# Optimization experiments

Measured on AMD Instinct MI355X. Metric: run time of the kernel, lower is better.

Reference implementation:

```python
import jax, jax.numpy as jnp
import numpy as np

N_NODES = 50000

def setup_inputs() -> dict:
    key = jax.random.key(0)
    k1, k2, k3, k4, k5 = jax.random.split(key, 5)
    x = jax.random.normal(k1, (50000, 128), dtype=jnp.float32)
    weight = jax.random.normal(k2, (128, 32), dtype=jnp.float32) * (np.sqrt(6.0 / (128 + 32)))
    edge_src = jax.random.randint(k3, (1600000,), 0, N_NODES, dtype=jnp.int32)
    edge_dst = jax.random.randint(k4, (1600000,), 0, N_NODES, dtype=jnp.int32)
    edge_weight = jax.random.uniform(k5, (1600000,), dtype=jnp.float32)
    return {"x": x, "weight": weight, "edge_src": edge_src,
            "edge_dst": edge_dst, "edge_weight": edge_weight}

def reference(x, weight, edge_src, edge_dst, edge_weight):
    # h = x @ W  (dense GEMM)
    h = x @ weight                                   # [N, out]
    # out = spmm(adj, h): gather h rows at src, scale by edge weight,
    # scatter-add into dst rows (COO SpMM).
    msgs = edge_weight[:, None] * h[edge_src]        # [E, out]
    out = jax.ops.segment_sum(msgs, edge_dst, num_segments=N_NODES)
    return out
```

## Files before the change

kernel.cpp:

```cpp
#include <hip/hip_runtime.h>
#include <hip/hip_bf16.h>
#include <stdint.h>

#define N_NODES   50000
#define K_DIM     128
#define OUT_DIM   32
#define N_EDGES   1600000
#define NBKT      782
#define CAP       3072
#define AFIT      16
#define FB        ((N_EDGES + 256*AFIT - 1) / (256*AFIT))
#define GB        ((N_NODES + 63) / 64)

__global__ __launch_bounds__(256) void zero_cursor(int* __restrict__ cursor) {
    for (int i = threadIdx.x; i < NBKT; i += 256) cursor[i] = 0;
}

__global__ __launch_bounds__(256) void gemm_fill(const float* __restrict__ x,
                                                 const float* __restrict__ w,
                                                 __hip_bfloat16* __restrict__ h,
                                                 const int*   __restrict__ esrc,
                                                 const int*   __restrict__ edst,
                                                 const float* __restrict__ ew,
                                                 int*         __restrict__ cursor,
                                                 uint64_t*    __restrict__ pairs) {
    __shared__ __align__(16) char smem[50176];
    const int t = threadIdx.x;

    if (blockIdx.x < FB) {
        int*      cnt   = (int*)smem;
        int*      wbase = (int*)(smem + 3200);
        int*      scr   = (int*)(smem + 6400);
        uint16_t* rkA   = (uint16_t*)(smem + 7424);
        uint64_t* stg   = (uint64_t*)(smem + 17408);

        for (int i = t; i < 800; i += 256) cnt[i] = 0;
        __syncthreads();

        uint32_t lo[AFIT], hi[AFIT];
        uint16_t rk[AFIT];
        const int base = blockIdx.x * 256 * AFIT;
        #pragma unroll
        for (int k = 0; k < AFIT; ++k) {
            const int e = base + k * 256 + t;
            if (e < N_EDGES) {
                const uint32_t s = (uint32_t)esrc[e];
                const uint32_t d = (uint32_t)edst[e];
                lo[k] = (d << 16) | s;
                hi[k] = __float_as_uint(ew[e]);
                rk[k] = (uint16_t)atomicAdd(&cnt[d >> 6], 1);
            } else {
                lo[k] = 0xffffffffu;
            }
        }
        __syncthreads();
        for (int i = t; i < NBKT; i += 256) {
            const int c = cnt[i];
            if (c) wbase[i] = atomicAdd(&cursor[i], c);
        }
        __syncthreads();
        int v0[4]; int lsum = 0;
        #pragma unroll
        for (int j = 0; j < 4; ++j) { v0[j] = cnt[t * 4 + j] * ((t * 4 + j) < 800); lsum += v0[j]; }
        scr[t] = lsum;
        __syncthreads();
        #pragma unroll
        for (int d = 1; d < 256; d <<= 1) {
            const int a = (t >= d) ? scr[t - d] : 0;
            __syncthreads();
            scr[t] += a;
            __syncthreads();
        }
        int run = scr[t] - lsum;
        #pragma unroll
        for (int j = 0; j < 4; ++j) {
            if (t * 4 + j < 800) { const int c = v0[j]; cnt[t * 4 + j] = run; run += c; }
        }
        __syncthreads();
        #pragma unroll
        for (int k = 0; k < AFIT; ++k) {
            if (lo[k] != 0xffffffffu) {
                const int b = (int)(lo[k] >> 22);
                const int i = cnt[b] + (int)rk[k];
                stg[i] = ((uint64_t)hi[k] << 32) | lo[k];
                rkA[i] = rk[k];
            }
        }
        __syncthreads();
        const int total = min(4096, N_EDGES - base);
        for (int i = t; i < total; i += 256) {
            const uint64_t p = stg[i];
            const int b    = (int)((p >> 22) & 0x3ff);
            const int gpos = wbase[b] + (int)rkA[i];
            if (gpos < CAP)
                pairs[(size_t)b * CAP + gpos] = p;
        }
    } else {
        float*  wlds = (float*)smem;
        float4* wl4  = (float4*)smem;
        float4* xl4  = (float4*)(smem + 16384);

        const float4* wg4 = reinterpret_cast<const float4*>(w);
        #pragma unroll
        for (int i = 0; i < 4; ++i) wl4[i * 256 + t] = wg4[i * 256 + t];

        const int row0 = (blockIdx.x - FB) * 64;
        const long long gbase4 = (long long)row0 * (K_DIM / 4);
        const long long gmax4  = (long long)N_NODES * (K_DIM / 4);
        const float4* xg4 = reinterpret_cast<const float4*>(x);
        #pragma unroll
        for (int i = 0; i < 8; ++i) {
            const int idx = i * 256 + t;
            const int row = idx >> 5;
            const int k4  = idx & 31;
            const long long gi = gbase4 + idx;
            xl4[row * 33 + k4] = (gi < gmax4) ? xg4[gi]
                                              : make_float4(0.f, 0.f, 0.f, 0.f);
        }
        __syncthreads();

        const int cg = t & 15;
        const int rg = t >> 4;
        const float2* w2 = reinterpret_cast<const float2*>(wlds);

        float acc[4][2] = {{0.f,0.f},{0.f,0.f},{0.f,0.f},{0.f,0.f}};
        #pragma unroll 4
        for (int k4 = 0; k4 < K_DIM / 4; ++k4) {
            const int k = k4 * 4;
            const float2 wv0 = w2[(k + 0) * 16 + cg];
            const float2 wv1 = w2[(k + 1) * 16 + cg];
            const float2 wv2 = w2[(k + 2) * 16 + cg];
            const float2 wv3 = w2[(k + 3) * 16 + cg];
            #pragma unroll
            for (int r = 0; r < 4; ++r) {
                const float4 xv = xl4[(rg * 4 + r) * 33 + k4];
                acc[r][0] += xv.x * wv0.x + xv.y * wv1.x + xv.z * wv2.x + xv.w * wv3.x;
                acc[r][1] += xv.x * wv0.y + xv.y * wv1.y + xv.z * wv2.y + xv.w * wv3.y;
            }
        }
        uint32_t* h32 = reinterpret_cast<uint32_t*>(h);
        #pragma unroll
        for (int r = 0; r < 4; ++r) {
            const int row = row0 + rg * 4 + r;
            if (row < N_NODES) {
                __hip_bfloat16 b0 = __float2bfloat16(acc[r][0]);
                __hip_bfloat16 b1 = __float2bfloat16(acc[r][1]);
                const uint32_t u0 = *reinterpret_cast<uint16_t*>(&b0);
                const uint32_t u1 = *reinterpret_cast<uint16_t*>(&b1);
                h32[row * 16 + cg] = u0 | (u1 << 16);
            }
        }
    }
}

__global__ __launch_bounds__(512) void sort_pull(const int*      __restrict__ cursor,
                                                 const uint64_t* __restrict__ pairs,
                                                 const __hip_bfloat16* __restrict__ h,
                                                 float*          __restrict__ out) {
    __shared__ uint64_t stg[CAP];
    __shared__ int lcnt[64];
    __shared__ int loff[65];
    const int b    = blockIdx.x;
    const int t    = threadIdx.x;
    const size_t beg = (size_t)b * CAP;
    const int cnt  = min(cursor[b], CAP);
    const int wv   = t >> 6;
    const int lane = t & 63;
    const int col  = lane & 31;
    const int half = lane >> 5;

    if (t < 64) lcnt[t] = 0;
    __syncthreads();

    uint64_t pl[6];
    int      pr[6];
    #pragma unroll
    for (int k = 0; k < 6; ++k) {
        const int i = t + k * 512;
        if (i < cnt) {
            const uint64_t p = pairs[beg + i];
            const int nl = (int)((p >> 16) & 63);
            pl[k] = p;
            pr[k] = (nl << 12) | atomicAdd(&lcnt[nl], 1);
        } else {
            pr[k] = -1;
        }
    }
    __syncthreads();
    if (t < 64) {
        const int v = lcnt[t];
        int p = v;
        #pragma unroll
        for (int d = 1; d < 64; d <<= 1) {
            const int n = __shfl_up(p, d, 64);
            if (t >= d) p += n;
        }
        loff[t] = p - v;
        if (t == 63) loff[64] = p;
    }
    __syncthreads();
    #pragma unroll
    for (int k = 0; k < 6; ++k) {
        if (pr[k] >= 0)
            stg[loff[pr[k] >> 12] + (pr[k] & 0xfff)] = pl[k];
    }
    __syncthreads();

    for (int nl = wv * 8; nl < wv * 8 + 8; ++nl) {
        const int node = (b << 6) + nl;
        if (node >= N_NODES) break;
        const int jb = loff[nl], je = loff[nl + 1];
        float acc = 0.f;
        int j = jb + half;
        for (; j + 6 < je; j += 8) {
            const uint64_t p0 = stg[j];
            const uint64_t p1 = stg[j + 2];
            const uint64_t p2 = stg[j + 4];
            const uint64_t p3 = stg[j + 6];
            const float a0 = __bfloat162float(h[(size_t)(p0 & 0xffffu) * OUT_DIM + col]);
            const float a1 = __bfloat162float(h[(size_t)(p1 & 0xffffu) * OUT_DIM + col]);
            const float a2 = __bfloat162float(h[(size_t)(p2 & 0xffffu) * OUT_DIM + col]);
            const float a3 = __bfloat162float(h[(size_t)(p3 & 0xffffu) * OUT_DIM + col]);
            acc += __uint_as_float((uint32_t)(p0 >> 32)) * a0;
            acc += __uint_as_float((uint32_t)(p1 >> 32)) * a1;
            acc += __uint_as_float((uint32_t)(p2 >> 32)) * a2;
            acc += __uint_as_float((uint32_t)(p3 >> 32)) * a3;
        }
        for (; j < je; j += 2) {
            const uint64_t p = stg[j];
            acc += __uint_as_float((uint32_t)(p >> 32)) *
                   __bfloat162float(h[(size_t)(p & 0xffffu) * OUT_DIM + col]);
        }
        acc += __shfl_xor(acc, 32, 64);
        if (half == 0) out[(size_t)node * OUT_DIM + col] = acc;
    }
}

__global__ __launch_bounds__(256) void gemm_only(const float* __restrict__ x,
                                                 const float* __restrict__ w,
                                                 __hip_bfloat16* __restrict__ h) {
    __shared__ float wlds[K_DIM * OUT_DIM];
    const int t = threadIdx.x;
    #pragma unroll
    for (int i = 0; i < (K_DIM * OUT_DIM) / 256; ++i)
        wlds[i * 256 + t] = w[i * 256 + t];
    __syncthreads();
    const int row = blockIdx.x * 8 + (t >> 5);
    const int col = t & 31;
    if (row >= N_NODES) return;
    const float4* x4 = reinterpret_cast<const float4*>(x + (size_t)row * K_DIM);
    float acc = 0.f;
    #pragma unroll
    for (int k4 = 0; k4 < K_DIM / 4; ++k4) {
        float4 xv = x4[k4];
        const int k = k4 * 4;
        acc += xv.x * wlds[(k + 0) * OUT_DIM + col] + xv.y * wlds[(k + 1) * OUT_DIM + col]
             + xv.z * wlds[(k + 2) * OUT_DIM + col] + xv.w * wlds[(k + 3) * OUT_DIM + col];
    }
    h[(size_t)row * OUT_DIM + col] = __float2bfloat16(acc);
}

__global__ __launch_bounds__(256) void scatter_kernel(const int*   __restrict__ esrc,
                                                      const int*   __restrict__ edst,
                                                      const float* __restrict__ ew,
                                                      const __hip_bfloat16* __restrict__ h,
                                                      float*       out) {
    const long long gid = (long long)blockIdx.x * blockDim.x + threadIdx.x;
    const int e   = (int)(gid >> 5);
    const int col = (int)(gid & 31);
    if (e >= N_EDGES) return;
    atomicAdd(out + (size_t)edst[e] * OUT_DIM + col,
              ew[e] * __bfloat162float(h[(size_t)esrc[e] * OUT_DIM + col]));
}

extern "C" void kernel_launch(void* const* d_in, const int* in_sizes, int n_in,
                              void* d_out, int out_size, void* d_ws, size_t ws_size,
                              hipStream_t stream) {
    const float* x    = (const float*)d_in[0];
    const float* w    = (const float*)d_in[1];
    const int*   esrc = (const int*)d_in[2];
    const int*   edst = (const int*)d_in[3];
    const float* ew   = (const float*)d_in[4];
    float*       out  = (float*)d_out;

    const size_t PAIRS_B = (size_t)NBKT * CAP * 8;
    const size_t H_B     = (size_t)N_NODES * OUT_DIM * 2;
    const size_t CUR_B   = (size_t)NBKT * 4;
    const size_t REQ     = PAIRS_B + H_B + CUR_B;

    uint64_t*        pairs  = (uint64_t*)d_ws;
    __hip_bfloat16*  h      = (__hip_bfloat16*)((char*)d_ws + PAIRS_B);
    int*             cursor = (int*)((char*)d_ws + PAIRS_B + H_B);

    if (ws_size >= REQ) {
        zero_cursor<<<1, 256, 0, stream>>>(cursor);
        gemm_fill<<<FB + GB, 256, 0, stream>>>(x, w, h, esrc, edst, ew, cursor, pairs);
        sort_pull<<<NBKT, 512, 0, stream>>>(cursor, pairs, h, out);
    } else {
        __hip_bfloat16* hf = (__hip_bfloat16*)d_ws;
        (void)hipMemsetAsync(d_out, 0, (size_t)out_size * sizeof(float), stream);
        gemm_only<<<(N_NODES + 7) / 8, 256, 0, stream>>>(x, w, hf);
        const long long total = (long long)N_EDGES * OUT_DIM;
        scatter_kernel<<<(int)((total + 255) / 256), 256, 0, stream>>>(esrc, edst, ew, hf, out);
    }
}
```

Baseline: 63.41 us.

## Use bf16 MFMA for the dense GEMM and shrink edge-binning tiles

Replaces the scalar FP32 FMA GEMM in the fused gemm_fill kernel with bf16 MFMA 16x16x32 instructions. x and W are converted to bf16 into padded LDS tiles first. The edge-binning blocks now process 8 edges per thread instead of 16, which doubles the number of binning blocks. Each edge's in-bucket rank is now recomputed from the prefix offsets instead of being stored in a separate LDS array. The shared memory footprint drops, which may allow more blocks per CU. In exchange, inputs are rounded to bf16 before the multiply, which lowers GEMM precision, and more blocks issue atomics on the global cursor.

```diff
diff --git a/kernel.cpp b/kernel.cpp
--- a/kernel.cpp
+++ b/kernel.cpp
@@ -8,9 +8,13 @@
 #define N_EDGES   1600000
 #define NBKT      782
 #define CAP       3072
-#define AFIT      16
+#define AFIT      8
 #define FB        ((N_EDGES + 256*AFIT - 1) / (256*AFIT))
 #define GB        ((N_NODES + 63) / 64)
+#define XSTR      136
+
+typedef __attribute__((ext_vector_type(8))) short bf16x8;
+typedef __attribute__((ext_vector_type(4))) float f32x4;
 
 __global__ __launch_bounds__(256) void zero_cursor(int* __restrict__ cursor) {
     for (int i = threadIdx.x; i < NBKT; i += 256) cursor[i] = 0;
@@ -24,15 +28,14 @@
                                                  const float* __restrict__ ew,
                                                  int*         __restrict__ cursor,
                                                  uint64_t*    __restrict__ pairs) {
-    __shared__ __align__(16) char smem[50176];
+    __shared__ __align__(16) char smem[26112];
     const int t = threadIdx.x;
 
     if (blockIdx.x < FB) {
         int*      cnt   = (int*)smem;
         int*      wbase = (int*)(smem + 3200);
         int*      scr   = (int*)(smem + 6400);
-        uint16_t* rkA   = (uint16_t*)(smem + 7424);
-        uint64_t* stg   = (uint64_t*)(smem + 17408);
+        uint64_t* stg   = (uint64_t*)(smem + 7424);
 
         for (int i = t; i < 800; i += 256) cnt[i] = 0;
         __syncthreads();
@@ -61,7 +64,7 @@
         __syncthreads();
         int v0[4]; int lsum = 0;
         #pragma unroll
-        for (int j = 0; j < 4; ++j) { v0[j] = cnt[t * 4 + j] * ((t * 4 + j) < 800); lsum += v0[j]; }
+        for (int j = 0; j < 4; ++j) { v0[j] = (t * 4 + j < 800) ? cnt[t * 4 + j] : 0; lsum += v0[j]; }
         scr[t] = lsum;
         __syncthreads();
         #pragma unroll
@@ -81,73 +84,72 @@
         for (int k = 0; k < AFIT; ++k) {
             if (lo[k] != 0xffffffffu) {
                 const int b = (int)(lo[k] >> 22);
-                const int i = cnt[b] + (int)rk[k];
-                stg[i] = ((uint64_t)hi[k] << 32) | lo[k];
-                rkA[i] = rk[k];
+                stg[cnt[b] + (int)rk[k]] = ((uint64_t)hi[k] << 32) | lo[k];
             }
         }
         __syncthreads();
-        const int total = min(4096, N_EDGES - base);
+        const int total = min(256 * AFIT, N_EDGES - base);
         for (int i = t; i < total; i += 256) {
             const uint64_t p = stg[i];
             const int b    = (int)((p >> 22) & 0x3ff);
-            const int gpos = wbase[b] + (int)rkA[i];
+            const int gpos = wbase[b] + i - cnt[b];
             if (gpos < CAP)
                 pairs[(size_t)b * CAP + gpos] = p;
         }
     } else {
-        float*  wlds = (float*)smem;
-        float4* wl4  = (float4*)smem;
-        float4* xl4  = (float4*)(smem + 16384);
-
-        const float4* wg4 = reinterpret_cast<const float4*>(w);
-        #pragma unroll
-        for (int i = 0; i < 4; ++i) wl4[i * 256 + t] = wg4[i * 256 + t];
-
+        uint16_t* wt = (uint16_t*)smem;
+        uint16_t* xt = (uint16_t*)(smem + 8704);
+
+        for (int i = t; i < K_DIM * OUT_DIM; i += 256) {
+            const int k = i >> 5, c = i & 31;
+            const __hip_bfloat16 bv = __float2bfloat16(w[i]);
+            wt[c * XSTR + k] = *(const uint16_t*)&bv;
+        }
         const int row0 = (blockIdx.x - FB) * 64;
-        const long long gbase4 = (long long)row0 * (K_DIM / 4);
-        const long long gmax4  = (long long)N_NODES * (K_DIM / 4);
         const float4* xg4 = reinterpret_cast<const float4*>(x);
+        const long long gmax4 = (long long)N_NODES * (K_DIM / 4);
         #pragma unroll
         for (int i = 0; i < 8; ++i) {
             const int idx = i * 256 + t;
             const int row = idx >> 5;
             const int k4  = idx & 31;
-            const long long gi = gbase4 + idx;
-            xl4[row * 33 + k4] = (gi < gmax4) ? xg4[gi]
-                                              : make_float4(0.f, 0.f, 0.f, 0.f);
-        }
-        __syncthreads();
-
-        const int cg = t & 15;
-        const int rg = t >> 4;
-        const float2* w2 = reinterpret_cast<const float2*>(wlds);
-
-        float acc[4][2] = {{0.f,0.f},{0.f,0.f},{0.f,0.f},{0.f,0.f}};
-        #pragma unroll 4
-        for (int k4 = 0; k4 < K_DIM / 4; ++k4) {
-            const int k = k4 * 4;
-            const float2 wv0 = w2[(k + 0) * 16 + cg];
-            const float2 wv1 = w2[(k + 1) * 16 + cg];
-            const float2 wv2 = w2[(k + 2) * 16 + cg];
-            const float2 wv3 = w2[(k + 3) * 16 + cg];
-            #pragma unroll
-            for (int r = 0; r < 4; ++r) {
-                const float4 xv = xl4[(rg * 4 + r) * 33 + k4];
-                acc[r][0] += xv.x * wv0.x + xv.y * wv1.x + xv.z * wv2.x + xv.w * wv3.x;
-                acc[r][1] += xv.x * wv0.y + xv.y * wv1.y + xv.z * wv2.y + xv.w * wv3.y;
-            }
-        }
-        uint32_t* h32 = reinterpret_cast<uint32_t*>(h);
+            const long long gi = (long long)(row0 + row) * (K_DIM / 4) + k4;
+            float4 v = make_float4(0.f, 0.f, 0.f, 0.f);
+            if (gi < gmax4) v = xg4[gi];
+            __hip_bfloat16 b0 = __float2bfloat16(v.x), b1 = __float2bfloat16(v.y);
+            __hip_bfloat16 b2 = __float2bfloat16(v.z), b3 = __float2bfloat16(v.w);
+            ushort4 u;
+            u.x = *(const uint16_t*)&b0; u.y = *(const uint16_t*)&b1;
+            u.z = *(const uint16_t*)&b2; u.w = *(const uint16_t*)&b3;
+            *reinterpret_cast<ushort4*>(xt + row * XSTR + k4 * 4) = u;
+        }
+        __syncthreads();
+
+        const int wv   = t >> 6;
+        const int lane = t & 63;
+        const int m    = lane & 15;
+        const int kg   = lane >> 4;
+
+        f32x4 acc0 = {0.f, 0.f, 0.f, 0.f};
+        f32x4 acc1 = {0.f, 0.f, 0.f, 0.f};
+        const uint16_t* arow = xt + (wv * 16 + m) * XSTR;
+        const uint16_t* b0p  = wt + m * XSTR;
+        const uint16_t* b1p  = wt + (16 + m) * XSTR;
+        #pragma unroll
+        for (int s = 0; s < 4; ++s) {
+            const int k0 = s * 32 + kg * 8;
+            const bf16x8 a  = *reinterpret_cast<const bf16x8*>(arow + k0);
+            const bf16x8 b0 = *reinterpret_cast<const bf16x8*>(b0p + k0);
+            const bf16x8 b1 = *reinterpret_cast<const bf16x8*>(b1p + k0);
+            acc0 = __builtin_amdgcn_mfma_f32_16x16x32_bf16(a, b0, acc0, 0, 0, 0);
+            acc1 = __builtin_amdgcn_mfma_f32_16x16x32_bf16(a, b1, acc1, 0, 0, 0);
+        }
         #pragma unroll
         for (int r = 0; r < 4; ++r) {
-            const int row = row0 + rg * 4 + r;
-            if (row < N_NODES) {
-                __hip_bfloat16 b0 = __float2bfloat16(acc[r][0]);
-                __hip_bfloat16 b1 = __float2bfloat16(acc[r][1]);
-                const uint32_t u0 = *reinterpret_cast<uint16_t*>(&b0);
-                const uint32_t u1 = *reinterpret_cast<uint16_t*>(&b1);
-                h32[row * 16 + cg] = u0 | (u1 << 16);
+            const int grow = row0 + wv * 16 + kg * 4 + r;
+            if (grow < N_NODES) {
+                h[(size_t)grow * OUT_DIM + m]      = __float2bfloat16(acc0[r]);
+                h[(size_t)grow * OUT_DIM + 16 + m] = __float2bfloat16(acc1[r]);
             }
         }
     }
```

After: 69.99 us. 1.1x slower.
